# Kernel tuning notes

Measured on AMD Instinct MI355X. Metric: run time of the kernel, lower is better.

The kernel has to match this reference:

```python
import jax, jax.numpy as jnp
import numpy as np

EPSILON = 1e-05
LOG_2PI = float(np.log(2.0 * np.pi))


def setup_inputs() -> dict:
    key = jax.random.key(0)
    k1, k2, k3 = jax.random.split(key, 3)
    B, S, K, N = 64, 1000, 12, 80  # batch, seq, n_states, n_channels
    x = jax.random.normal(k1, (B, S, N), dtype=jnp.float32)
    mu = jax.random.normal(k2, (B, K, N), dtype=jnp.float32)
    # Positive-definite covariances per (batch, state)
    A = jax.random.normal(k3, (B, K, N, N), dtype=jnp.float32)
    sigma = A @ jnp.swapaxes(A, -1, -2) / N + jnp.eye(N, dtype=jnp.float32)
    return {"x": x, "mu": mu, "sigma": sigma}


def reference(x, mu, sigma):
    """Batched-over-states MVN log-likelihood.

    x: (B, S, N); mu: (B, K, N); sigma: (B, K, N, N).
    Returns log_likelihood: (B, S, K).
    """
    N = x.shape[-1]
    # add_epsilon with diag=True: epsilon * I on the diagonal
    sigma = sigma + jnp.asarray(EPSILON, sigma.dtype) * jnp.eye(N, dtype=sigma.dtype)
    L = jnp.linalg.cholesky(sigma)  # (B, K, N, N), batched across states
    diff = x[:, :, None, :] - mu[:, None, :, :]  # (B, S, K, N)
    # Solve L z = diff, batched: L -> (B, 1, K, N, N), diff -> (B, S, K, N, 1)
    z = jax.scipy.linalg.solve_triangular(L[:, None], diff[..., None], lower=True)[..., 0]
    quad = jnp.sum(z * z, axis=-1)  # (B, S, K)
    logdet_half = jnp.sum(jnp.log(jnp.diagonal(L, axis1=-2, axis2=-1)), axis=-1)  # (B, K)
    ll = -0.5 * quad - logdet_half[:, None, :] - 0.5 * N * jnp.asarray(LOG_2PI, x.dtype)
    return ll  # (B, S, K)
```

## Files before the change

### kernel.cpp

```cpp
#include <hip/hip_runtime.h>

#define Bb 64
#define Ss 1000
#define Kk 12
#define Nn 80
#define CTERM 73.51508265637381f
#define STA 84

typedef __attribute__((ext_vector_type(8))) short short8;
typedef __attribute__((ext_vector_type(4))) float f32x4;

static __device__ __forceinline__ unsigned short f2bf(float f) {
    unsigned u = __builtin_bit_cast(unsigned, f);
    unsigned r = u + 0x7FFFu + ((u >> 16) & 1u);
    return (unsigned short)(r >> 16);
}

__global__ __launch_bounds__(512, 6) void prep_kernel(
    const float* __restrict__ sigma, const float* __restrict__ mu,
    const float* __restrict__ x,
    uint4* __restrict__ wsWh,
    float* __restrict__ wsV, float* __restrict__ wsL,
    uint4* __restrict__ Xh, int doX)
{
    __shared__ float Ls[Nn * STA];
    __shared__ float invd[Nn];
    __shared__ float mus[Nn];
    __shared__ float ldp[8];
    __shared__ float vps[8 * Nn];

    const int bk  = blockIdx.x;
    const int tid = threadIdx.x;
    const int w   = tid >> 6;
    const int l   = tid & 63;
    const int r2  = l + 64;

    const float4* sp4 = (const float4*)(sigma + (size_t)bk * Nn * Nn);
    #pragma unroll
    for (int it = 0; it < 4; ++it) {
        int ci = tid + 512 * it;
        if (ci < 1600) {
            int r = ci / 20, c4 = 4 * (ci - 20 * r);
            if (c4 <= r + 3) {
                float4 v = sp4[ci];
                *(float4*)&Ls[r * STA + c4] = v;
            }
        }
    }
    if (tid < Nn) mus[tid] = mu[(size_t)bk * Nn + tid];
    __syncthreads();
    if (tid < Nn) Ls[tid * STA + tid] += 1e-5f;
    __syncthreads();

    float ldacc = 0.0f;
    for (int p = 0; p < 20; ++p) {
        const int j0 = 4 * p;
        const bool a1 = (l >= j0);
        const bool a2 = (l < 16) && (r2 >= j0);

        if (w == (p & 7)) {
            float B00 = Ls[j0*STA+j0];
            float B10 = Ls[(j0+1)*STA+j0], B11 = Ls[(j0+1)*STA+j0+1];
            float B20 = Ls[(j0+2)*STA+j0], B21 = Ls[(j0+2)*STA+j0+1], B22 = Ls[(j0+2)*STA+j0+2];
            float B30 = Ls[(j0+3)*STA+j0], B31 = Ls[(j0+3)*STA+j0+1], B32 = Ls[(j0+3)*STA+j0+2], B33 = Ls[(j0+3)*STA+j0+3];
            float rv0 = rsqrtf(B00);
            float l10 = B10*rv0, l20 = B20*rv0, l30 = B30*rv0;
            float t11 = fmaf(-l10,l10,B11);                    float rv1 = rsqrtf(t11);
            float l21 = fmaf(-l20,l10,B21)*rv1;
            float l31 = fmaf(-l30,l10,B31)*rv1;
            float t22 = fmaf(-l21,l21,fmaf(-l20,l20,B22));     float rv2 = rsqrtf(t22);
            float l32 = fmaf(-l31,l21,fmaf(-l30,l20,B32))*rv2;
            float t33 = fmaf(-l32,l32,fmaf(-l31,l31,fmaf(-l30,l30,B33)));
            float rv3 = rsqrtf(t33);
            ldacc += 0.5f * (logf(B00) + logf(t11) + logf(t22) + logf(t33));
            if (l == 0) { invd[j0]=rv0; invd[j0+1]=rv1; invd[j0+2]=rv2; invd[j0+3]=rv3; }

            if (a1) {
                float4 a = *(float4*)&Ls[l * STA + j0];
                float b0 = a.x * rv0;
                float b1 = fmaf(-l10, b0, a.y) * rv1;
                float b2 = fmaf(-l21, b1, fmaf(-l20, b0, a.z)) * rv2;
                float b3 = fmaf(-l32, b2, fmaf(-l31, b1, fmaf(-l30, b0, a.w))) * rv3;
                *(float4*)&Ls[l * STA + j0] = make_float4(b0, b1, b2, b3);
            }
            if (a2) {
                float4 a = *(float4*)&Ls[r2 * STA + j0];
                float c0 = a.x * rv0;
                float c1 = fmaf(-l10, c0, a.y) * rv1;
                float c2 = fmaf(-l21, c1, fmaf(-l20, c0, a.z)) * rv2;
                float c3 = fmaf(-l32, c2, fmaf(-l31, c1, fmaf(-l30, c0, a.w))) * rv3;
                *(float4*)&Ls[r2 * STA + j0] = make_float4(c0, c1, c2, c3);
            }
        }
        __syncthreads();

        const int gs0 = p + 1;
        const int g0 = gs0 + ((w - gs0) & 7);
        #pragma unroll 2
        for (int g = g0; g < 20; g += 8) {
            const int cb = 4 * g;
            float4 q0 = *(const float4*)&Ls[(cb+0) * STA + j0];
            float4 q1 = *(const float4*)&Ls[(cb+1) * STA + j0];
            float4 q2 = *(const float4*)&Ls[(cb+2) * STA + j0];
            float4 q3 = *(const float4*)&Ls[(cb+3) * STA + j0];
            {
                const int R = cb + l;
                if (R < Nn) {
                    float4 pv = *(const float4*)&Ls[R * STA + j0];
                    float4 t  = *(float4*)&Ls[R * STA + cb];
                    t.x = fmaf(-pv.x,q0.x, fmaf(-pv.y,q0.y, fmaf(-pv.z,q0.z, fmaf(-pv.w,q0.w, t.x))));
                    t.y = fmaf(-pv.x,q1.x, fmaf(-pv.y,q1.y, fmaf(-pv.z,q1.z, fmaf(-pv.w,q1.w, t.y))));
                    t.z = fmaf(-pv.x,q2.x, fmaf(-pv.y,q2.y, fmaf(-pv.z,q2.z, fmaf(-pv.w,q2.w, t.z))));
                    t.w = fmaf(-pv.x,q3.x, fmaf(-pv.y,q3.y, fmaf(-pv.z,q3.z, fmaf(-pv.w,q3.w, t.w))));
                    *(float4*)&Ls[R * STA + cb] = t;
                }
            }
            if (cb + 64 < Nn) {
                const int R = cb + 64 + l;
                if (R < Nn) {
                    float4 pv = *(const float4*)&Ls[R * STA + j0];
                    float4 t  = *(float4*)&Ls[R * STA + cb];
                    t.x = fmaf(-pv.x,q0.x, fmaf(-pv.y,q0.y, fmaf(-pv.z,q0.z, fmaf(-pv.w,q0.w, t.x))));
                    t.y = fmaf(-pv.x,q1.x, fmaf(-pv.y,q1.y, fmaf(-pv.z,q1.z, fmaf(-pv.w,q1.w, t.y))));
                    t.z = fmaf(-pv.x,q2.x, fmaf(-pv.y,q2.y, fmaf(-pv.z,q2.z, fmaf(-pv.w,q2.w, t.z))));
                    t.w = fmaf(-pv.x,q3.x, fmaf(-pv.y,q3.y, fmaf(-pv.z,q3.z, fmaf(-pv.w,q3.w, t.w))));
                    *(float4*)&Ls[R * STA + cb] = t;
                }
            }
        }
    }
    if (l == 0) ldp[w] = ldacc;
    __syncthreads();
    if (tid == 0) wsL[bk] = ldp[0]+ldp[1]+ldp[2]+ldp[3]+ldp[4]+ldp[5]+ldp[6]+ldp[7];

    for (int i = tid; i < Nn * Nn; i += 512) {
        int r = i / Nn, c = i - Nn * r;
        if (c > r) Ls[r * STA + c] = 0.0f;
    }
    __syncthreads();

    for (int p = 0; p < 20; ++p) {
        const int i0 = 4 * p;
        const bool b1a = (i0 + 3 >= l);
        const bool b2a = (l < 16) && (i0 + 3 >= r2);

        if (w == (p & 7)) {
            float m10 = Ls[(i0+1)*STA + i0];
            float m20 = Ls[(i0+2)*STA + i0];
            float m30 = Ls[(i0+3)*STA + i0];
            float m21 = Ls[(i0+2)*STA + i0+1];
            float m31 = Ls[(i0+3)*STA + i0+1];
            float m32 = Ls[(i0+3)*STA + i0+2];
            float4 iv = *(const float4*)&invd[i0];
            if (b1a) {
                float4 a = *(float4*)&Ls[l * STA + i0];
                if (l >= i0)
                    a = make_float4(l==i0?1.f:0.f, l==i0+1?1.f:0.f, l==i0+2?1.f:0.f, l==i0+3?1.f:0.f);
                float w0 = a.x * iv.x;
                float w1 = fmaf(-w0, m10, a.y) * iv.y;
                float w2 = fmaf(-w1, m21, fmaf(-w0, m20, a.z)) * iv.z;
                float w3 = fmaf(-w2, m32, fmaf(-w1, m31, fmaf(-w0, m30, a.w))) * iv.w;
                *(float4*)&Ls[l * STA + i0] = make_float4(w0, w1, w2, w3);
            }
            if (b2a) {
                float4 a = *(float4*)&Ls[r2 * STA + i0];
                if (r2 >= i0)
                    a = make_float4(r2==i0?1.f:0.f, r2==i0+1?1.f:0.f, r2==i0+2?1.f:0.f, r2==i0+3?1.f:0.f);
                float v0 = a.x * iv.x;
                float v1 = fmaf(-v0, m10, a.y) * iv.y;
                float v2 = fmaf(-v1, m21, fmaf(-v0, m20, a.z)) * iv.z;
                float v3 = fmaf(-v2, m32, fmaf(-v1, m31, fmaf(-v0, m30, a.w))) * iv.w;
                *(float4*)&Ls[r2 * STA + i0] = make_float4(v0, v1, v2, v3);
            }
        }
        __syncthreads();

        float4 wv = make_float4(0.f,0.f,0.f,0.f), vv = make_float4(0.f,0.f,0.f,0.f);
        if (b1a) wv = *(float4*)&Ls[l * STA + i0];
        if (b2a) vv = *(float4*)&Ls[r2 * STA + i0];
        if (b1a | b2a) {
            const int gs0 = p + 1;
            const int g0 = gs0 + ((w - gs0) & 7);
            for (int g = g0; g < 20; g += 8) {
                float4 q0 = *(const float4*)&Ls[(4*g+0) * STA + i0];
                float4 q1 = *(const float4*)&Ls[(4*g+1) * STA + i0];
                float4 q2 = *(const float4*)&Ls[(4*g+2) * STA + i0];
                float4 q3 = *(const float4*)&Ls[(4*g+3) * STA + i0];
                if (b1a) {
                    float4 t = *(float4*)&Ls[l * STA + 4*g];
                    t.x = fmaf(-wv.x,q0.x, fmaf(-wv.y,q0.y, fmaf(-wv.z,q0.z, fmaf(-wv.w,q0.w, t.x))));
                    t.y = fmaf(-wv.x,q1.x, fmaf(-wv.y,q1.y, fmaf(-wv.z,q1.z, fmaf(-wv.w,q1.w, t.y))));
                    t.z = fmaf(-wv.x,q2.x, fmaf(-wv.y,q2.y, fmaf(-wv.z,q2.z, fmaf(-wv.w,q2.w, t.z))));
                    t.w = fmaf(-wv.x,q3.x, fmaf(-wv.y,q3.y, fmaf(-wv.z,q3.z, fmaf(-wv.w,q3.w, t.w))));
                    *(float4*)&Ls[l * STA + 4*g] = t;
                }
                if (b2a) {
                    float4 t = *(float4*)&Ls[r2 * STA + 4*g];
                    t.x = fmaf(-vv.x,q0.x, fmaf(-vv.y,q0.y, fmaf(-vv.z,q0.z, fmaf(-vv.w,q0.w, t.x))));
                    t.y = fmaf(-vv.x,q1.x, fmaf(-vv.y,q1.y, fmaf(-vv.z,q1.z, fmaf(-vv.w,q1.w, t.y))));
                    t.z = fmaf(-vv.x,q2.x, fmaf(-vv.y,q2.y, fmaf(-vv.z,q2.z, fmaf(-vv.w,q2.w, t.z))));
                    t.w = fmaf(-vv.x,q3.x, fmaf(-vv.y,q3.y, fmaf(-vv.z,q3.z, fmaf(-vv.w,q3.w, t.w))));
                    *(float4*)&Ls[r2 * STA + 4*g] = t;
                }
            }
        }
    }
    __syncthreads();

    {
        float s1 = 0.f, s2 = 0.f;
        const int c0 = 10 * w;
        #pragma unroll 2
        for (int cc = 0; cc < 10; ++cc) {
            int c = c0 + cc;
            float mc = mus[c];
            float e1 = (c <= l)  ? Ls[c * STA + l]  : 0.f;
            s1 = fmaf(e1, mc, s1);
            if (l < 16) {
                float e2 = (c <= r2) ? Ls[c * STA + r2] : 0.f;
                s2 = fmaf(e2, mc, s2);
            }
        }
        vps[w * Nn + l] = s1;
        if (l < 16) vps[w * Nn + r2] = s2;
        __syncthreads();
        if (tid < Nn) {
            float acc = 0.f;
            #pragma unroll
            for (int ww = 0; ww < 8; ++ww) acc += vps[ww * Nn + tid];
            wsV[(size_t)bk * Nn + tid] = acc;
        }
    }

    const int n = l & 15, quad = l >> 4;
    uint4* ph = wsWh + (size_t)bk * 800;
    for (int f = w; f < 10; f += 8) {
        int ks = f / 5, mt = f - 5 * ks;
        int m = 16 * mt + n, kb = 32 * ks + 8 * quad;
        unsigned hh[8];
        #pragma unroll
        for (int j = 0; j < 8; ++j) {
            float wj = (m >= kb + j) ? Ls[(kb + j) * STA + m] : 0.f;
            hh[j] = f2bf(wj);
        }
        ph[f*64 + l] = make_uint4(hh[0]|(hh[1]<<16), hh[2]|(hh[3]<<16), hh[4]|(hh[5]<<16), hh[6]|(hh[7]<<16));
    }
    if (w < 5) {
        int mt = w;
        if (quad < 2) {
            int m = 16 * mt + n, kb = 64 + 8 * quad;
            unsigned hh[8];
            #pragma unroll
            for (int j = 0; j < 8; ++j) {
                float wj = (m >= kb + j) ? Ls[(kb + j) * STA + m] : 0.f;
                hh[j] = f2bf(wj);
            }
            ph[640 + mt*32 + l] = make_uint4(hh[0]|(hh[1]<<16), hh[2]|(hh[3]<<16), hh[4]|(hh[5]<<16), hh[6]|(hh[7]<<16));
        }
    }

    if (doX) {
        const int wid = bk * 8 + w;
        const int qd = l >> 4, n2 = l & 15;
        #pragma unroll
        for (int it = 0; it < 2; ++it) {
            int G = wid + 6144 * it;
            if (G >= 12096) break;
            int b2  = G / 189;
            int rem = G - b2 * 189;
            int sg  = rem / 3, ks = rem - 3 * sg;
            int s   = sg * 16 + n2;
            int k0  = 32 * ks + 8 * qd;
            float d[8] = {0.f,0.f,0.f,0.f,0.f,0.f,0.f,0.f};
            if (s < Ss) {
                const float* xp = x + ((size_t)b2 * Ss + s) * Nn + k0;
                float4 f0 = *(const float4*)xp;
                float4 f1 = *(const float4*)(xp + 4);
                d[0]=f0.x; d[1]=f0.y; d[2]=f0.z; d[3]=f0.w;
                d[4]=f1.x; d[5]=f1.y; d[6]=f1.z; d[7]=f1.w;
            }
            unsigned hh[8];
            #pragma unroll
            for (int j = 0; j < 8; ++j) hh[j] = f2bf(d[j]);
            size_t slot = ((size_t)(b2 * 64 + sg) * 3 + ks) * 64 + l;
            Xh[slot] = make_uint4(hh[0]|(hh[1]<<16), hh[2]|(hh[3]<<16), hh[4]|(hh[5]<<16), hh[6]|(hh[7]<<16));
        }
    }
}

__global__ __launch_bounds__(512) void ll_kernel2(
    const uint4* __restrict__ Xh,
    const uint4* __restrict__ wsWh,
    const float* __restrict__ wsV, const float* __restrict__ wsL,
    float* __restrict__ out)
{
    __shared__ uint4 WhL[960];
    const int b = blockIdx.x;
    const int k = blockIdx.y;
    const int bk = b * Kk + k;
    const int tid = threadIdx.x;
    const int wv = tid >> 6, lane = tid & 63;
    const int n = lane & 15, quad = lane >> 4;

    const uint4* gh = wsWh + (size_t)bk * 800;
    #pragma unroll
    for (int it = 0; it < 2; ++it) {
        int i = tid + 512 * it;
        if (i < 640) WhL[i] = gh[i];
    }
    if (tid < 320) {
        int mt = tid >> 6, ln = tid & 63, qd = (ln >> 4);
        uint4 vh = make_uint4(0,0,0,0);
        if (qd < 2) vh = gh[640 + mt*32 + ln];
        WhL[640 + tid] = vh;
    }
    __syncthreads();

    const float ld = wsL[bk];
    f32x4 vf[5];
    #pragma unroll
    for (int mt = 0; mt < 5; ++mt)
        vf[mt] = *(const f32x4*)&wsV[(size_t)bk * Nn + 16*mt + 4*quad];

    for (int it = 0; it < 4; ++it) {
        const int sg0 = wv * 8 + it * 2;
        short8 bh[2][3];
        #pragma unroll
        for (int t = 0; t < 2; ++t)
            #pragma unroll
            for (int ks = 0; ks < 3; ++ks) {
                size_t base = ((size_t)(b * 64 + sg0 + t) * 3 + ks) * 64 + lane;
                bh[t][ks] = __builtin_bit_cast(short8, Xh[base]);
            }

        f32x4 acc[2][5];
        #pragma unroll
        for (int t = 0; t < 2; ++t)
            #pragma unroll
            for (int mt = 0; mt < 5; ++mt) acc[t][mt] = (f32x4){0.f,0.f,0.f,0.f};

        #pragma unroll
        for (int ks = 0; ks < 3; ++ks) {
            #pragma unroll
            for (int mt = 0; mt < 5; ++mt) {
                const int fi = (ks < 2) ? (ks*5 + mt)*64 + lane : 640 + mt*64 + lane;
                short8 wh = __builtin_bit_cast(short8, WhL[fi]);
                #pragma unroll
                for (int t = 0; t < 2; ++t)
                    acc[t][mt] = __builtin_amdgcn_mfma_f32_16x16x32_bf16(wh, bh[t][ks], acc[t][mt], 0, 0, 0);
            }
        }

        #pragma unroll
        for (int t = 0; t < 2; ++t) {
            float q2 = 0.f;
            #pragma unroll
            for (int mt = 0; mt < 5; ++mt)
                #pragma unroll
                for (int r = 0; r < 4; ++r) {
                    float y = acc[t][mt][r] - vf[mt][r];
                    q2 = fmaf(y, y, q2);
                }
            q2 += __shfl_xor(q2, 16, 64);
            q2 += __shfl_xor(q2, 32, 64);
            int gs = (sg0 + t) * 16 + n;
            if (lane < 16 && gs < Ss)
                out[((size_t)b * Ss + gs) * Kk + k] = -0.5f * q2 - ld - CTERM;
        }
    }
}

__global__ __launch_bounds__(256) void ll_kernel(
    const float* __restrict__ x,
    const uint4* __restrict__ wsWh,
    const float* __restrict__ wsV, const float* __restrict__ wsL,
    float* __restrict__ out)
{
    const int b    = blockIdx.x;
    const int st   = blockIdx.y;
    const int tid  = threadIdx.x;
    const int wv   = tid >> 6, lane = tid & 63;
    const int n    = lane & 15, quad = lane >> 4;
    const int sbase = st * 128 + wv * 32;

    short8 xh[2][3];
    #pragma unroll
    for (int t = 0; t < 2; ++t) {
        int gs = sbase + 16 * t + n;
        #pragma unroll
        for (int ks = 0; ks < 3; ++ks) {
            int kb = 32 * ks + 8 * quad;
            float d[8] = {0.f,0.f,0.f,0.f,0.f,0.f,0.f,0.f};
            if (gs < Ss && kb < Nn) {
                const float* xp = x + ((size_t)b * Ss + gs) * Nn + kb;
                float4 f0 = *(const float4*)xp;
                float4 f1 = *(const float4*)(xp + 4);
                d[0]=f0.x; d[1]=f0.y; d[2]=f0.z; d[3]=f0.w;
                d[4]=f1.x; d[5]=f1.y; d[6]=f1.z; d[7]=f1.w;
            }
            short8 h;
            #pragma unroll
            for (int j = 0; j < 8; ++j) h[j] = (short)f2bf(d[j]);
            xh[t][ks] = h;
        }
    }

    for (int k = 0; k < Kk; ++k) {
        const int bk = b * Kk + k;
        const uint4* ah_p = wsWh + (size_t)bk * 800;

        f32x4 acc[2][5];
        #pragma unroll
        for (int t = 0; t < 2; ++t)
            #pragma unroll
            for (int mt = 0; mt < 5; ++mt) acc[t][mt] = (f32x4){0.f,0.f,0.f,0.f};

        #pragma unroll
        for (int ks = 0; ks < 3; ++ks) {
            short8 ah[5];
            if (ks < 2) {
                #pragma unroll
                for (int mt = 0; mt < 5; ++mt)
                    ah[mt] = __builtin_bit_cast(short8, ah_p[(ks*5 + mt)*64 + lane]);
            } else {
                #pragma unroll
                for (int mt = 0; mt < 5; ++mt) {
                    uint4 zh = make_uint4(0,0,0,0);
                    if (quad < 2) zh = ah_p[640 + mt*32 + lane];
                    ah[mt] = __builtin_bit_cast(short8, zh);
                }
            }
            #pragma unroll
            for (int mt = 0; mt < 5; ++mt)
                #pragma unroll
                for (int t = 0; t < 2; ++t)
                    acc[t][mt] = __builtin_amdgcn_mfma_f32_16x16x32_bf16(ah[mt], xh[t][ks], acc[t][mt], 0, 0, 0);
        }

        float ld = wsL[bk];
        f32x4 vf[5];
        #pragma unroll
        for (int mt = 0; mt < 5; ++mt)
            vf[mt] = *(const f32x4*)&wsV[(size_t)bk * Nn + 16*mt + 4*quad];
        #pragma unroll
        for (int t = 0; t < 2; ++t) {
            float q2 = 0.f;
            #pragma unroll
            for (int mt = 0; mt < 5; ++mt)
                #pragma unroll
                for (int r = 0; r < 4; ++r) {
                    float y = acc[t][mt][r] - vf[mt][r];
                    q2 = fmaf(y, y, q2);
                }
            q2 += __shfl_xor(q2, 16, 64);
            q2 += __shfl_xor(q2, 32, 64);
            int gs = sbase + 16 * t + n;
            if (lane < 16 && gs < Ss)
                out[((size_t)b * Ss + gs) * Kk + k] = -0.5f * q2 - ld - CTERM;
        }
    }
}

#define ST1 81
__global__ __launch_bounds__(256) void mvn_ll_fallback(
    const float* __restrict__ x, const float* __restrict__ mu,
    const float* __restrict__ sigma, float* __restrict__ out)
{
    __shared__ float Ls[Nn * ST1];
    __shared__ float invd[Nn];
    __shared__ float mus[Nn];
    __shared__ float logdet_s;

    const int bk = blockIdx.x, b = bk / Kk, k = bk - b * Kk;
    const int tid = threadIdx.x, nt = blockDim.x;

    const float* sp = sigma + (size_t)bk * Nn * Nn;
    for (int t = tid; t < Nn * Nn; t += nt) Ls[(t / Nn) * ST1 + (t % Nn)] = sp[t];
    if (tid < Nn) mus[tid] = mu[(size_t)bk * Nn + tid];
    __syncthreads();
    if (tid < Nn) Ls[tid * ST1 + tid] += 1e-5f;
    __syncthreads();
    for (int j = 0; j < Nn; ++j) {
        if (tid == 0) {
            float d = sqrtf(Ls[j * ST1 + j]);
            Ls[j * ST1 + j] = d; invd[j] = 1.0f / d;
        }
        __syncthreads();
        const float inv = invd[j];
        for (int i = j + 1 + tid; i < Nn; i += nt) Ls[i * ST1 + j] *= inv;
        __syncthreads();
        for (int t = tid; t < Nn * Nn; t += nt) {
            int r = t / Nn, c = t % Nn;
            if (r > j && c > j && c <= r)
                Ls[r * ST1 + c] -= Ls[r * ST1 + j] * Ls[c * ST1 + j];
        }
        __syncthreads();
    }
    if (tid == 0) {
        float a = 0.f; for (int j = 0; j < Nn; ++j) a += logf(Ls[j * ST1 + j]);
        logdet_s = a;
    }
    __syncthreads();
    const float ld = logdet_s;
    for (int s = tid; s < Ss; s += nt) {
        const float4* xp = (const float4*)(x + ((size_t)b * Ss + s) * Nn);
        float a[Nn];
        #pragma unroll
        for (int q = 0; q < Nn / 4; ++q) {
            float4 v = xp[q];
            a[4*q+0] = v.x - mus[4*q+0]; a[4*q+1] = v.y - mus[4*q+1];
            a[4*q+2] = v.z - mus[4*q+2]; a[4*q+3] = v.w - mus[4*q+3];
        }
        #pragma unroll
        for (int i = 0; i < Nn; ++i) {
            float t = a[i];
            #pragma unroll
            for (int j = 0; j < i; ++j) t = fmaf(-Ls[i * ST1 + j], a[j], t);
            a[i] = t * invd[i];
        }
        float quad = 0.f;
        #pragma unroll
        for (int i = 0; i < Nn; ++i) quad = fmaf(a[i], a[i], quad);
        out[((size_t)b * Ss + s) * Kk + k] = -0.5f * quad - ld - CTERM;
    }
}

extern "C" void kernel_launch(void* const* d_in, const int* in_sizes, int n_in,
                              void* d_out, int out_size, void* d_ws, size_t ws_size,
                              hipStream_t stream) {
    const float* x     = (const float*)d_in[0];
    const float* mu    = (const float*)d_in[1];
    const float* sigma = (const float*)d_in[2];
    float* out = (float*)d_out;

    const size_t nBK   = (size_t)Bb * Kk;
    const size_t nWu4  = nBK * 800;
    const size_t nXu4  = (size_t)Bb * 64 * 3 * 64;
    const size_t need_mid  = nWu4 * 16 + nBK * Nn * 4 + nBK * 4;
    const size_t need_full = need_mid + nXu4 * 16;

    if (ws_size >= need_full) {
        uint4* wsWh = (uint4*)d_ws;
        uint4* Xh   = wsWh + nWu4;
        float* wsV  = (float*)(Xh + nXu4);
        float* wsL  = wsV + nBK * Nn;
        prep_kernel<<<dim3(Bb * Kk), dim3(512), 0, stream>>>(
            sigma, mu, x, wsWh, wsV, wsL, Xh, 1);
        ll_kernel2<<<dim3(Bb, Kk), dim3(512), 0, stream>>>(Xh, wsWh, wsV, wsL, out);
    } else if (ws_size >= need_mid) {
        uint4* wsWh = (uint4*)d_ws;
        float* wsV  = (float*)(wsWh + nWu4);
        float* wsL  = wsV + nBK * Nn;
        prep_kernel<<<dim3(Bb * Kk), dim3(512), 0, stream>>>(
            sigma, mu, x, wsWh, wsV, wsL, (uint4*)nullptr, 0);
        ll_kernel<<<dim3(Bb, 8), dim3(256), 0, stream>>>(x, wsWh, wsV, wsL, out);
    } else {
        mvn_ll_fallback<<<dim3(Bb * Kk), dim3(256), 0, stream>>>(x, mu, sigma, out);
    }
}
```

Before: 140.5 us.

## Fuse Cholesky factorization and triangular inversion into one skewed blocked loop

Merges the blocked Cholesky loop and the separate in-place triangular inverse loop into a single loop of 21 steps. The inverse of panel p-1 now runs alongside the factorization of panel p, so the two phases share one barrier per step instead of two loops each with their own barriers. The pass that zeroed the upper triangle is removed; identity and zero values are synthesized in registers instead of being read from the upper part. This roughly halves the barrier count in the prep kernel, at the cost of more complex per-step control flow and a correctness risk if the two concurrent phases touch overlapping shared-memory blocks.

```diff
diff --git a/kernel.cpp b/kernel.cpp
--- a/kernel.cpp
+++ b/kernel.cpp
@@ -53,12 +53,11 @@
     __syncthreads();
 
     float ldacc = 0.0f;
-    for (int p = 0; p < 20; ++p) {
+    for (int p = 0; p <= 20; ++p) {
         const int j0 = 4 * p;
-        const bool a1 = (l >= j0);
-        const bool a2 = (l < 16) && (r2 >= j0);
-
-        if (w == (p & 7)) {
+        const int i0 = 4 * (p - 1);
+
+        if (p < 20 && w == (p & 7)) {
             float B00 = Ls[j0*STA+j0];
             float B10 = Ls[(j0+1)*STA+j0], B11 = Ls[(j0+1)*STA+j0+1];
             float B20 = Ls[(j0+2)*STA+j0], B21 = Ls[(j0+2)*STA+j0+1], B22 = Ls[(j0+2)*STA+j0+2];
@@ -75,7 +74,7 @@
             ldacc += 0.5f * (logf(B00) + logf(t11) + logf(t22) + logf(t33));
             if (l == 0) { invd[j0]=rv0; invd[j0+1]=rv1; invd[j0+2]=rv2; invd[j0+3]=rv3; }
 
-            if (a1) {
+            if (l >= j0) {
                 float4 a = *(float4*)&Ls[l * STA + j0];
                 float b0 = a.x * rv0;
                 float b1 = fmaf(-l10, b0, a.y) * rv1;
@@ -83,7 +82,7 @@
                 float b3 = fmaf(-l32, b2, fmaf(-l31, b1, fmaf(-l30, b0, a.w))) * rv3;
                 *(float4*)&Ls[l * STA + j0] = make_float4(b0, b1, b2, b3);
             }
-            if (a2) {
+            if (l < 16 && r2 >= j0) {
                 float4 a = *(float4*)&Ls[r2 * STA + j0];
                 float c0 = a.x * rv0;
                 float c1 = fmaf(-l10, c0, a.y) * rv1;
@@ -92,59 +91,8 @@
                 *(float4*)&Ls[r2 * STA + j0] = make_float4(c0, c1, c2, c3);
             }
         }
-        __syncthreads();
-
-        const int gs0 = p + 1;
-        const int g0 = gs0 + ((w - gs0) & 7);
-        #pragma unroll 2
-        for (int g = g0; g < 20; g += 8) {
-            const int cb = 4 * g;
-            float4 q0 = *(const float4*)&Ls[(cb+0) * STA + j0];
-            float4 q1 = *(const float4*)&Ls[(cb+1) * STA + j0];
-            float4 q2 = *(const float4*)&Ls[(cb+2) * STA + j0];
-            float4 q3 = *(const float4*)&Ls[(cb+3) * STA + j0];
-            {
-                const int R = cb + l;
-                if (R < Nn) {
-                    float4 pv = *(const float4*)&Ls[R * STA + j0];
-                    float4 t  = *(float4*)&Ls[R * STA + cb];
-                    t.x = fmaf(-pv.x,q0.x, fmaf(-pv.y,q0.y, fmaf(-pv.z,q0.z, fmaf(-pv.w,q0.w, t.x))));
-                    t.y = fmaf(-pv.x,q1.x, fmaf(-pv.y,q1.y, fmaf(-pv.z,q1.z, fmaf(-pv.w,q1.w, t.y))));
-                    t.z = fmaf(-pv.x,q2.x, fmaf(-pv.y,q2.y, fmaf(-pv.z,q2.z, fmaf(-pv.w,q2.w, t.z))));
-                    t.w = fmaf(-pv.x,q3.x, fmaf(-pv.y,q3.y, fmaf(-pv.z,q3.z, fmaf(-pv.w,q3.w, t.w))));
-                    *(float4*)&Ls[R * STA + cb] = t;
-                }
-            }
-            if (cb + 64 < Nn) {
-                const int R = cb + 64 + l;
-                if (R < Nn) {
-                    float4 pv = *(const float4*)&Ls[R * STA + j0];
-                    float4 t  = *(float4*)&Ls[R * STA + cb];
-                    t.x = fmaf(-pv.x,q0.x, fmaf(-pv.y,q0.y, fmaf(-pv.z,q0.z, fmaf(-pv.w,q0.w, t.x))));
-                    t.y = fmaf(-pv.x,q1.x, fmaf(-pv.y,q1.y, fmaf(-pv.z,q1.z, fmaf(-pv.w,q1.w, t.y))));
-                    t.z = fmaf(-pv.x,q2.x, fmaf(-pv.y,q2.y, fmaf(-pv.z,q2.z, fmaf(-pv.w,q2.w, t.z))));
-                    t.w = fmaf(-pv.x,q3.x, fmaf(-pv.y,q3.y, fmaf(-pv.z,q3.z, fmaf(-pv.w,q3.w, t.w))));
-                    *(float4*)&Ls[R * STA + cb] = t;
-                }
-            }
-        }
-    }
-    if (l == 0) ldp[w] = ldacc;
-    __syncthreads();
-    if (tid == 0) wsL[bk] = ldp[0]+ldp[1]+ldp[2]+ldp[3]+ldp[4]+ldp[5]+ldp[6]+ldp[7];
-
-    for (int i = tid; i < Nn * Nn; i += 512) {
-        int r = i / Nn, c = i - Nn * r;
-        if (c > r) Ls[r * STA + c] = 0.0f;
-    }
-    __syncthreads();
-
-    for (int p = 0; p < 20; ++p) {
-        const int i0 = 4 * p;
-        const bool b1a = (i0 + 3 >= l);
-        const bool b2a = (l < 16) && (i0 + 3 >= r2);
-
-        if (w == (p & 7)) {
+
+        if (p >= 1 && w == ((p - 1) & 7)) {
             float m10 = Ls[(i0+1)*STA + i0];
             float m20 = Ls[(i0+2)*STA + i0];
             float m30 = Ls[(i0+3)*STA + i0];
@@ -152,20 +100,24 @@
             float m31 = Ls[(i0+3)*STA + i0+1];
             float m32 = Ls[(i0+3)*STA + i0+2];
             float4 iv = *(const float4*)&invd[i0];
-            if (b1a) {
-                float4 a = *(float4*)&Ls[l * STA + i0];
+            if (i0 + 3 >= l) {
+                float4 a;
                 if (l >= i0)
                     a = make_float4(l==i0?1.f:0.f, l==i0+1?1.f:0.f, l==i0+2?1.f:0.f, l==i0+3?1.f:0.f);
+                else
+                    a = *(float4*)&Ls[l * STA + i0];
                 float w0 = a.x * iv.x;
                 float w1 = fmaf(-w0, m10, a.y) * iv.y;
                 float w2 = fmaf(-w1, m21, fmaf(-w0, m20, a.z)) * iv.z;
                 float w3 = fmaf(-w2, m32, fmaf(-w1, m31, fmaf(-w0, m30, a.w))) * iv.w;
                 *(float4*)&Ls[l * STA + i0] = make_float4(w0, w1, w2, w3);
             }
-            if (b2a) {
-                float4 a = *(float4*)&Ls[r2 * STA + i0];
+            if (l < 16 && i0 + 3 >= r2) {
+                float4 a;
                 if (r2 >= i0)
                     a = make_float4(r2==i0?1.f:0.f, r2==i0+1?1.f:0.f, r2==i0+2?1.f:0.f, r2==i0+3?1.f:0.f);
+                else
+                    a = *(float4*)&Ls[r2 * STA + i0];
                 float v0 = a.x * iv.x;
                 float v1 = fmaf(-v0, m10, a.y) * iv.y;
                 float v2 = fmaf(-v1, m21, fmaf(-v0, m20, a.z)) * iv.z;
@@ -175,36 +127,84 @@
         }
         __syncthreads();
 
-        float4 wv = make_float4(0.f,0.f,0.f,0.f), vv = make_float4(0.f,0.f,0.f,0.f);
-        if (b1a) wv = *(float4*)&Ls[l * STA + i0];
-        if (b2a) vv = *(float4*)&Ls[r2 * STA + i0];
-        if (b1a | b2a) {
+        if (p < 20) {
             const int gs0 = p + 1;
             const int g0 = gs0 + ((w - gs0) & 7);
             for (int g = g0; g < 20; g += 8) {
-                float4 q0 = *(const float4*)&Ls[(4*g+0) * STA + i0];
-                float4 q1 = *(const float4*)&Ls[(4*g+1) * STA + i0];
-                float4 q2 = *(const float4*)&Ls[(4*g+2) * STA + i0];
-                float4 q3 = *(const float4*)&Ls[(4*g+3) * STA + i0];
-                if (b1a) {
-                    float4 t = *(float4*)&Ls[l * STA + 4*g];
-                    t.x = fmaf(-wv.x,q0.x, fmaf(-wv.y,q0.y, fmaf(-wv.z,q0.z, fmaf(-wv.w,q0.w, t.x))));
-                    t.y = fmaf(-wv.x,q1.x, fmaf(-wv.y,q1.y, fmaf(-wv.z,q1.z, fmaf(-wv.w,q1.w, t.y))));
-                    t.z = fmaf(-wv.x,q2.x, fmaf(-wv.y,q2.y, fmaf(-wv.z,q2.z, fmaf(-wv.w,q2.w, t.z))));
-                    t.w = fmaf(-wv.x,q3.x, fmaf(-wv.y,q3.y, fmaf(-wv.z,q3.z, fmaf(-wv.w,q3.w, t.w))));
-                    *(float4*)&Ls[l * STA + 4*g] = t;
+                const int cb = 4 * g;
+                float4 q0 = *(const float4*)&Ls[(cb+0) * STA + j0];
+                float4 q1 = *(const float4*)&Ls[(cb+1) * STA + j0];
+                float4 q2 = *(const float4*)&Ls[(cb+2) * STA + j0];
+                float4 q3 = *(const float4*)&Ls[(cb+3) * STA + j0];
+                {
+                    const int R = cb + l;
+                    if (R < Nn) {
+                        float4 pv = *(const float4*)&Ls[R * STA + j0];
+                        float4 t  = *(float4*)&Ls[R * STA + cb];
+                        t.x = fmaf(-pv.x,q0.x, fmaf(-pv.y,q0.y, fmaf(-pv.z,q0.z, fmaf(-pv.w,q0.w, t.x))));
+                        t.y = fmaf(-pv.x,q1.x, fmaf(-pv.y,q1.y, fmaf(-pv.z,q1.z, fmaf(-pv.w,q1.w, t.y))));
+                        t.z = fmaf(-pv.x,q2.x, fmaf(-pv.y,q2.y, fmaf(-pv.z,q2.z, fmaf(-pv.w,q2.w, t.z))));
+                        t.w = fmaf(-pv.x,q3.x, fmaf(-pv.y,q3.y, fmaf(-pv.z,q3.z, fmaf(-pv.w,q3.w, t.w))));
+                        *(float4*)&Ls[R * STA + cb] = t;
+                    }
                 }
-                if (b2a) {
-                    float4 t = *(float4*)&Ls[r2 * STA + 4*g];
-                    t.x = fmaf(-vv.x,q0.x, fmaf(-vv.y,q0.y, fmaf(-vv.z,q0.z, fmaf(-vv.w,q0.w, t.x))));
-                    t.y = fmaf(-vv.x,q1.x, fmaf(-vv.y,q1.y, fmaf(-vv.z,q1.z, fmaf(-vv.w,q1.w, t.y))));
-                    t.z = fmaf(-vv.x,q2.x, fmaf(-vv.y,q2.y, fmaf(-vv.z,q2.z, fmaf(-vv.w,q2.w, t.z))));
-                    t.w = fmaf(-vv.x,q3.x, fmaf(-vv.y,q3.y, fmaf(-vv.z,q3.z, fmaf(-vv.w,q3.w, t.w))));
-                    *(float4*)&Ls[r2 * STA + 4*g] = t;
+                if (cb + 64 < Nn) {
+                    const int R = cb + 64 + l;
+                    if (R < Nn) {
+                        float4 pv = *(const float4*)&Ls[R * STA + j0];
+                        float4 t  = *(float4*)&Ls[R * STA + cb];
+                        t.x = fmaf(-pv.x,q0.x, fmaf(-pv.y,q0.y, fmaf(-pv.z,q0.z, fmaf(-pv.w,q0.w, t.x))));
+                        t.y = fmaf(-pv.x,q1.x, fmaf(-pv.y,q1.y, fmaf(-pv.z,q1.z, fmaf(-pv.w,q1.w, t.y))));
+                        t.z = fmaf(-pv.x,q2.x, fmaf(-pv.y,q2.y, fmaf(-pv.z,q2.z, fmaf(-pv.w,q2.w, t.z))));
+                        t.w = fmaf(-pv.x,q3.x, fmaf(-pv.y,q3.y, fmaf(-pv.z,q3.z, fmaf(-pv.w,q3.w, t.w))));
+                        *(float4*)&Ls[R * STA + cb] = t;
+                    }
                 }
             }
         }
-    }
+
+        if (p >= 1) {
+            const bool b1a = (i0 + 3 >= l);
+            const bool b2a = (l < 16) && (i0 + 3 >= r2);
+            if (b1a | b2a) {
+                float4 wv = make_float4(0.f,0.f,0.f,0.f), vv = make_float4(0.f,0.f,0.f,0.f);
+                if (b1a) wv = *(float4*)&Ls[l * STA + i0];
+                if (b2a) vv = *(float4*)&Ls[r2 * STA + i0];
+                const int gs0 = p;
+                const int g0 = gs0 + ((w - gs0) & 7);
+                for (int g = g0; g < 20; g += 8) {
+                    const int cb = 4 * g;
+                    float4 q0 = *(const float4*)&Ls[(cb+0) * STA + i0];
+                    float4 q1 = *(const float4*)&Ls[(cb+1) * STA + i0];
+                    float4 q2 = *(const float4*)&Ls[(cb+2) * STA + i0];
+                    float4 q3 = *(const float4*)&Ls[(cb+3) * STA + i0];
+                    if (b1a) {
+                        float4 t;
+                        if (l >= i0) t = make_float4(0.f, 0.f, 0.f, 0.f);
+                        else         t = *(float4*)&Ls[l * STA + cb];
+                        t.x = fmaf(-wv.x,q0.x, fmaf(-wv.y,q0.y, fmaf(-wv.z,q0.z, fmaf(-wv.w,q0.w, t.x))));
+                        t.y = fmaf(-wv.x,q1.x, fmaf(-wv.y,q1.y, fmaf(-wv.z,q1.z, fmaf(-wv.w,q1.w, t.y))));
+                        t.z = fmaf(-wv.x,q2.x, fmaf(-wv.y,q2.y, fmaf(-wv.z,q2.z, fmaf(-wv.w,q2.w, t.z))));
+                        t.w = fmaf(-wv.x,q3.x, fmaf(-wv.y,q3.y, fmaf(-wv.z,q3.z, fmaf(-wv.w,q3.w, t.w))));
+                        *(float4*)&Ls[l * STA + cb] = t;
+                    }
+                    if (b2a) {
+                        float4 t;
+                        if (r2 >= i0) t = make_float4(0.f, 0.f, 0.f, 0.f);
+                        else          t = *(float4*)&Ls[r2 * STA + cb];
+                        t.x = fmaf(-vv.x,q0.x, fmaf(-vv.y,q0.y, fmaf(-vv.z,q0.z, fmaf(-vv.w,q0.w, t.x))));
+                        t.y = fmaf(-vv.x,q1.x, fmaf(-vv.y,q1.y, fmaf(-vv.z,q1.z, fmaf(-vv.w,q1.w, t.y))));
+                        t.z = fmaf(-vv.x,q2.x, fmaf(-vv.y,q2.y, fmaf(-vv.z,q2.z, fmaf(-vv.w,q2.w, t.z))));
+                        t.w = fmaf(-vv.x,q3.x, fmaf(-vv.y,q3.y, fmaf(-vv.z,q3.z, fmaf(-vv.w,q3.w, t.w))));
+                        *(float4*)&Ls[r2 * STA + cb] = t;
+                    }
+                }
+            }
+        }
+    }
+    if (l == 0) ldp[w] = ldacc;
+    __syncthreads();
+    if (tid == 0) wsL[bk] = ldp[0]+ldp[1]+ldp[2]+ldp[3]+ldp[4]+ldp[5]+ldp[6]+ldp[7];
     __syncthreads();
 
     {
```

Result: no change. 138.8 us (-1.2%).
